# Performance work log

Measured on AMD Instinct MI355X. Metric: run time of the kernel, lower is better.

The kernel has to match this reference:

```python
import jax, jax.numpy as jnp
import numpy as np
import math

DEPTH = 3
NUM_GRAPHS = 8
BN_EPS = 1e-5
POOL_RATIO = 0.5


def _gcn(A, x, W, b):
    # GCNConv(improved=True): A_hat = A + 2*I; out = D^-1/2 A_hat D^-1/2 (x W) + b
    n = A.shape[0]
    A_hat = A + 2.0 * jnp.eye(n, dtype=A.dtype)
    deg = A_hat.sum(axis=1)
    d = jnp.where(deg > 0, jax.lax.rsqrt(deg), 0.0)
    return d[:, None] * (A_hat @ (d[:, None] * (x @ W))) + b


def _bn_eval(x, g, b):
    # BatchNorm1d in eval mode with running_mean=0, running_var=1
    return x * (g / jnp.sqrt(1.0 + BN_EPS)) + b


def _forward(x, edge_index, batch, conv0_w, conv0_b, down_w, down_b, pool_w,
             up_w, up_b, lins_w, lins_b, bn_g, bn_b, out_w, out_b):
    n0 = x.shape[0]
    # dense weighted adjacency A[dst, src] += 1 (duplicates sum, same as scatter-add MP)
    A = jnp.zeros((n0, n0), x.dtype).at[edge_index[1], edge_index[0]].add(1.0)

    # ---- GraphUNet (eval mode: dropout p=0.92 is identity) ----
    h = jax.nn.relu(_gcn(A, x, conv0_w, conv0_b))
    xs, As, perms = [h], [A], []
    for i in range(DEPTH):
        n = A.shape[0]
        eye = jnp.eye(n, dtype=A.dtype)
        S = A + eye                       # add_self_loops(weight=1)
        A2 = (S @ S) * (1.0 - eye)        # spspmm then remove_self_loops
        # TopKPooling: score = tanh((x.w)/||w||), keep top ceil(0.5*n) nodes
        score = jnp.tanh((h @ pool_w[i]) / jnp.linalg.norm(pool_w[i]))
        k = math.ceil(POOL_RATIO * n)
        _, perm = jax.lax.top_k(score, k)
        h = h[perm] * score[perm][:, None]
        A = A2[perm][:, perm]             # filter_adj
        h = jax.nn.relu(_gcn(A, h, down_w[i], down_b[i]))
        if i < DEPTH - 1:
            xs.append(h)
            As.append(A)
        perms.append(perm)
    for i in range(DEPTH):
        j = DEPTH - 1 - i
        res, Aj, perm = xs[j], As[j], perms[j]
        up = jnp.zeros_like(res).at[perm].set(h)
        h = res + up                      # sum_res=True skip connection
        h = _gcn(Aj, h, up_w[i], up_b[i])
        if i < DEPTH - 1:
            h = jax.nn.relu(h)

    # ---- global_add_pool + BN/Linear/tanh head ----
    g = jax.ops.segment_sum(h, batch, num_segments=NUM_GRAPHS)
    for i in range(3):
        g = _bn_eval(g, bn_g[i], bn_b[i])
        g = jnp.tanh(g @ lins_w[i] + lins_b[i])
    g = _bn_eval(g, bn_g[3], bn_b[3])
    return g @ out_w + out_b


def setup_inputs() -> dict:
    key = jax.random.key(0)
    ks = jax.random.split(key, 20)
    N, F, H, O, E = 4096, 64, 128, 32, 65536
    s = 0.05
    x = jax.random.normal(ks[0], (N, F), jnp.float32)
    src = jax.random.randint(ks[1], (E,), 0, N)
    dst = jax.random.randint(ks[2], (E,), 0, N)
    edge_index = jnp.stack([jnp.concatenate([src, dst]),
                            jnp.concatenate([dst, src])]).astype(jnp.int32)
    batch = jnp.sort(jax.random.randint(ks[3], (N,), 0, NUM_GRAPHS)).astype(jnp.int32)
    return {
        "x": x,
        "edge_index": edge_index,
        "batch": batch,
        "conv0_w": jax.random.normal(ks[4], (F, H), jnp.float32) * s,
        "conv0_b": jnp.zeros((H,), jnp.float32),
        "down_w": jax.random.normal(ks[5], (DEPTH, H, H), jnp.float32) * s,
        "down_b": jnp.zeros((DEPTH, H), jnp.float32),
        "pool_w": jax.random.normal(ks[6], (DEPTH, H), jnp.float32),
        "up_w": jax.random.normal(ks[7], (DEPTH, H, H), jnp.float32) * s,
        "up_b": jnp.zeros((DEPTH, H), jnp.float32),
        "lins_w": jax.random.normal(ks[8], (3, H, H), jnp.float32) * s,
        "lins_b": jnp.zeros((3, H), jnp.float32),
        "bn_g": jnp.ones((4, H), jnp.float32),
        "bn_b": jnp.zeros((4, H), jnp.float32),
        "out_w": jax.random.normal(ks[9], (H, O), jnp.float32) * s,
        "out_b": jnp.zeros((O,), jnp.float32),
    }


def reference(x, edge_index, batch, conv0_w, conv0_b, down_w, down_b, pool_w,
              up_w, up_b, lins_w, lins_b, bn_g, bn_b, out_w, out_b):
    return _forward(x, edge_index, batch, conv0_w, conv0_b, down_w, down_b,
                    pool_w, up_w, up_b, lins_w, lins_b, bn_g, bn_b, out_w, out_b)
```

## Files before the change

### kernel.cpp

```cpp
#include <hip/hip_runtime.h>
#include <math.h>

#define H 128
#define NG 8

typedef __attribute__((ext_vector_type(8))) short bf16x8;
typedef __attribute__((ext_vector_type(8))) unsigned short ushort8;
typedef __attribute__((ext_vector_type(4))) float f32x4;

static __device__ __forceinline__ float b2f(unsigned short u) {
  union { unsigned int i; float f; } v;
  v.i = ((unsigned int)u) << 16;
  return v.f;
}
static __device__ __forceinline__ unsigned short f2b(float f) {
  return (unsigned short)(__float_as_uint(f) >> 16);
}

__global__ void k_hist(const int* __restrict__ ei, int E, int* __restrict__ cnt) {
  int e = blockIdx.x * 256 + threadIdx.x;
  if (e >= E) return;
  atomicAdd(&cnt[ei[E + e]], 1);
}

__global__ __launch_bounds__(1024) void k_scan(const int* __restrict__ cnt,
                                               int* __restrict__ rowptr, int n) {
  __shared__ int sums[1024];
  int tid = threadIdx.x;
  int base = tid * 4;
  int v0 = 0, v1 = 0, v2 = 0, v3 = 0;
  if (base < n) { v0 = cnt[base]; v1 = cnt[base + 1]; v2 = cnt[base + 2]; v3 = cnt[base + 3]; }
  int s = v0 + v1 + v2 + v3;
  sums[tid] = s;
  __syncthreads();
  for (int off = 1; off < 1024; off <<= 1) {
    int t = (tid >= off) ? sums[tid - off] : 0;
    __syncthreads();
    sums[tid] += t;
    __syncthreads();
  }
  int excl = sums[tid] - s;
  if (base < n) {
    rowptr[base] = excl;
    rowptr[base + 1] = excl + v0;
    rowptr[base + 2] = excl + v0 + v1;
    rowptr[base + 3] = excl + v0 + v1 + v2;
  }
  if (tid == 1023) rowptr[n] = sums[1023];
}

__global__ void k_fill(const int* __restrict__ ei, int E, const int* __restrict__ rowptr,
                       int* __restrict__ cursor, int* __restrict__ colidx) {
  int e = blockIdx.x * 256 + threadIdx.x;
  if (e >= E) return;
  int r = ei[E + e], c = ei[e];
  int p = atomicAdd(&cursor[r], 1);
  colidx[rowptr[r] + p] = c;
}

__global__ void k_dvcnt(const int* __restrict__ cnt, float* __restrict__ dv, int n) {
  int i = blockIdx.x * 256 + threadIdx.x;
  if (i < n) dv[i] = rsqrtf((float)cnt[i] + 2.0f);
}

__global__ void k_deg(const float* __restrict__ A, int n, float* __restrict__ dv) {
  int row = blockIdx.x * (blockDim.x >> 6) + (threadIdx.x >> 6);
  int lane = threadIdx.x & 63;
  if (row >= n) return;
  float s = 0.f;
  const float* arow = A + (size_t)row * n;
  for (int j = lane; j < n; j += 64) s += arow[j];
#pragma unroll
  for (int o = 32; o > 0; o >>= 1) s += __shfl_down(s, o);
  if (lane == 0) dv[row] = rsqrtf(s + 2.0f);
}

template <int MODE>
__global__ __launch_bounds__(256) void k_xw(const float* __restrict__ X,
                                            const float* __restrict__ W,
                                            const float* __restrict__ dv,
                                            const int* __restrict__ idx,
                                            const float* __restrict__ aux,
                                            float* __restrict__ Y, int n, int F) {
  __shared__ float Xs[64][36];
  __shared__ float Ws[32][132];
  __shared__ int ridx[64];
  __shared__ float rscl[64];
  int tid = threadIdx.x;
  int rowBase = blockIdx.x * 64;
  if (MODE == 1) {
    if (tid < 64) {
      int pp = idx[rowBase + tid];
      ridx[tid] = pp;
      rscl[tid] = aux[pp];
    }
  } else if (MODE == 2) {
    if (tid < 64) ridx[tid] = idx[rowBase + tid];
  }
  if (MODE != 0) __syncthreads();
  int r0 = (tid >> 5) << 3;
  int c0 = (tid & 31) << 2;
  float acc[8][4] = {};
  for (int k0 = 0; k0 < F; k0 += 32) {
#pragma unroll
    for (int it = 0, e = tid; it < 8; ++it, e += 256) {
      int ii = e >> 5, kk = e & 31;
      int gk = k0 + kk;
      float v;
      if (MODE == 0) {
        v = X[(size_t)(rowBase + ii) * F + gk];
      } else if (MODE == 1) {
        v = X[(size_t)ridx[ii] * F + gk] * rscl[ii];
      } else {
        v = X[(size_t)(rowBase + ii) * F + gk];
        int iv = ridx[ii];
        if (iv >= 0) v += aux[(size_t)iv * H + gk];
      }
      Xs[ii][kk] = v;
    }
#pragma unroll
    for (int it = 0, e = tid; it < 4; ++it, e += 256) {
      int kk = e >> 5, cc4 = e & 31;
      *(float4*)&Ws[kk][cc4 << 2] = *(const float4*)&W[(size_t)(k0 + kk) * H + (cc4 << 2)];
    }
    __syncthreads();
#pragma unroll
    for (int kk = 0; kk < 32; kk += 4) {
      float4 a4[8], w4[4];
#pragma unroll
      for (int i = 0; i < 8; ++i) a4[i] = *(const float4*)&Xs[r0 + i][kk];
#pragma unroll
      for (int s = 0; s < 4; ++s) w4[s] = *(const float4*)&Ws[kk + s][c0];
#pragma unroll
      for (int i = 0; i < 8; ++i) {
        float av[4] = {a4[i].x, a4[i].y, a4[i].z, a4[i].w};
#pragma unroll
        for (int s = 0; s < 4; ++s) {
          float wv[4] = {w4[s].x, w4[s].y, w4[s].z, w4[s].w};
#pragma unroll
          for (int j = 0; j < 4; ++j) acc[i][j] = fmaf(av[s], wv[j], acc[i][j]);
        }
      }
    }
    __syncthreads();
  }
#pragma unroll
  for (int i = 0; i < 8; ++i) {
    int row = rowBase + r0 + i;
    float d = dv[row];
    *(float4*)&Y[(size_t)row * H + c0] =
        make_float4(d * acc[i][0], d * acc[i][1], d * acc[i][2], d * acc[i][3]);
  }
}

__global__ void k_spmm_fin(const int* __restrict__ rowptr, const int* __restrict__ colidx,
                           const float* __restrict__ Y, const float* __restrict__ dv,
                           const float* __restrict__ bias, float* __restrict__ Out,
                           int n, int relu) {
  int row = blockIdx.x * 4 + (threadIdx.x >> 6);
  int lane = threadIdx.x & 63;
  if (row >= n) return;
  int s = rowptr[row], e = rowptr[row + 1];
  float a0 = 0.f, a1 = 0.f;
  int i = s;
  for (; i + 1 < e; i += 2) {
    int c0 = colidx[i], c1 = colidx[i + 1];
    a0 += Y[(size_t)c0 * H + lane] + Y[(size_t)c1 * H + lane];
    a1 += Y[(size_t)c0 * H + 64 + lane] + Y[(size_t)c1 * H + 64 + lane];
  }
  if (i < e) {
    int c = colidx[i];
    a0 += Y[(size_t)c * H + lane];
    a1 += Y[(size_t)c * H + 64 + lane];
  }
  float d = dv[row];
  float v0 = d * (a0 + 2.0f * Y[(size_t)row * H + lane]) + bias[lane];
  float v1 = d * (a1 + 2.0f * Y[(size_t)row * H + 64 + lane]) + bias[64 + lane];
  if (relu) { v0 = fmaxf(v0, 0.f); v1 = fmaxf(v1, 0.f); }
  Out[(size_t)row * H + lane] = v0;
  Out[(size_t)row * H + 64 + lane] = v1;
}

__global__ __launch_bounds__(256) void k_ata_rows(const int* __restrict__ rowptr,
                                                  const int* __restrict__ colidx,
                                                  const int* __restrict__ perm,
                                                  const int* __restrict__ inv,
                                                  unsigned short* __restrict__ Ab,
                                                  float* __restrict__ dv, int kdim) {
  __shared__ int acc[2048];
  __shared__ int wsum[4];
  int i = blockIdx.x;
  int tid = threadIdx.x;
  for (int j = tid; j < kdim; j += 256) acc[j] = 0;
  __syncthreads();
  int p = perm[i];
  int s = rowptr[p], e = rowptr[p + 1];
  int deg = e - s;
  int wave = tid >> 6, lane = tid & 63;
  for (int q = wave; q <= deg; q += 4) {
    int kn = (q < deg) ? colidx[s + q] : p;
    int s2 = rowptr[kn], e2 = rowptr[kn + 1];
    for (int idx = s2 + lane; idx <= e2; idx += 64) {
      int j = (idx < e2) ? colidx[idx] : kn;
      int ii = inv[j];
      if (ii >= 0) atomicAdd(&acc[ii], 1);
    }
  }
  __syncthreads();
  int rs = 0;
  {
    int j0 = tid * 8;
    ushort8 v;
#pragma unroll
    for (int q = 0; q < 8; ++q) {
      int j = j0 + q;
      int c = (j == i) ? 0 : acc[j];
      rs += c;
      v[q] = f2b((float)c);
    }
    *(ushort8*)&Ab[(size_t)i * kdim + j0] = v;
  }
#pragma unroll
  for (int o = 32; o > 0; o >>= 1) rs += __shfl_down(rs, o);
  if (lane == 0) wsum[wave] = rs;
  __syncthreads();
  if (tid == 0) dv[i] = rsqrtf((float)(wsum[0] + wsum[1] + wsum[2] + wsum[3]) + 2.0f);
}

__global__ void k_gather(const unsigned short* __restrict__ Ab, const int* __restrict__ perm,
                         unsigned short* __restrict__ P, int n, int k) {
  int row = blockIdx.x;
  int p = perm[row];
  const unsigned short* src = Ab + (size_t)p * n;
  unsigned short* dst = P + (size_t)row * n;
  for (int c = threadIdx.x * 8; c < n; c += 256 * 8) {
    *(ushort8*)&dst[c] = *(const ushort8*)&src[c];
  }
  __syncthreads();
  if (threadIdx.x == 0) dst[p] = f2b(b2f(src[p]) + 1.0f);
}

__global__ __launch_bounds__(256) void k_ata_mfma(const unsigned short* __restrict__ P,
                                                  float* __restrict__ C, int n, int k) {
  __shared__ __align__(16) unsigned short As[64][64];
  __shared__ __align__(16) unsigned short Bs[64][64];
  int tid = threadIdx.x;
  int w = tid >> 6, ln = tid & 63;
  int l15 = ln & 15, l4 = ln >> 4;
  int br = blockIdx.y, bc = blockIdx.x;
  f32x4 acc[4] = {};
  for (int k0 = 0; k0 < n; k0 += 64) {
#pragma unroll
    for (int it = 0; it < 2; ++it) {
      int e = tid + it * 256;
      int row = e >> 3, ch = e & 7;
      int sch = (ch ^ (row & 7)) * 8;
      *(ushort8*)&As[row][sch] = *(const ushort8*)&P[(size_t)(br * 64 + row) * n + k0 + ch * 8];
      *(ushort8*)&Bs[row][sch] = *(const ushort8*)&P[(size_t)(bc * 64 + row) * n + k0 + ch * 8];
    }
    __syncthreads();
#pragma unroll
    for (int s = 0; s < 2; ++s) {
      int arow = w * 16 + l15;
      bf16x8 af = *(const bf16x8*)&As[arow][((s * 4 + l4) ^ (arow & 7)) * 8];
#pragma unroll
      for (int f = 0; f < 4; ++f) {
        int brow = f * 16 + l15;
        bf16x8 bfr = *(const bf16x8*)&Bs[brow][((s * 4 + l4) ^ (brow & 7)) * 8];
        acc[f] = __builtin_amdgcn_mfma_f32_16x16x32_bf16(af, bfr, acc[f], 0, 0, 0);
      }
    }
    __syncthreads();
  }
#pragma unroll
  for (int f = 0; f < 4; ++f) {
#pragma unroll
    for (int r = 0; r < 4; ++r) {
      int gi = br * 64 + w * 16 + l4 * 4 + r;
      int gj = bc * 64 + f * 16 + l15;
      C[(size_t)gi * k + gj] = (gi == gj) ? 0.0f : acc[f][r];
    }
  }
}

__global__ __launch_bounds__(256) void k_ata_sk(const float* __restrict__ A,
                                                const int* __restrict__ perm,
                                                float* __restrict__ C, int n, int k, int CK) {
  int bc = blockIdx.x, br = blockIdx.y;
  if (br > bc) return;
  __shared__ float As[64][36];
  __shared__ float Bs[64][36];
  __shared__ int pr[64], pc[64];
  int tid = threadIdx.x;
  if (tid < 64) pr[tid] = perm[br * 64 + tid];
  else if (tid < 128) pc[tid - 64] = perm[bc * 64 + (tid - 64)];
  __syncthreads();
  int ty = tid >> 4;
  int tx = tid & 15;
  float acc[4][4] = {};
  int k0s = blockIdx.z * CK;
  for (int k0 = k0s; k0 < k0s + CK; k0 += 32) {
#pragma unroll
    for (int it = 0, e = tid; it < 8; ++it, e += 256) {
      int ii = e >> 5, kk = e & 31;
      int gk = k0 + kk;
      int p = pr[ii];
      As[ii][kk] = A[(size_t)p * n + gk] + ((p == gk) ? 1.0f : 0.0f);
      p = pc[ii];
      Bs[ii][kk] = A[(size_t)p * n + gk] + ((p == gk) ? 1.0f : 0.0f);
    }
    __syncthreads();
#pragma unroll
    for (int kk = 0; kk < 32; kk += 4) {
      float4 a4[4], b4[4];
#pragma unroll
      for (int i = 0; i < 4; ++i) a4[i] = *(const float4*)&As[ty + 16 * i][kk];
#pragma unroll
      for (int j = 0; j < 4; ++j) b4[j] = *(const float4*)&Bs[tx + 16 * j][kk];
#pragma unroll
      for (int i = 0; i < 4; ++i) {
        float av[4] = {a4[i].x, a4[i].y, a4[i].z, a4[i].w};
#pragma unroll
        for (int j = 0; j < 4; ++j) {
          float bv[4] = {b4[j].x, b4[j].y, b4[j].z, b4[j].w};
#pragma unroll
          for (int s = 0; s < 4; ++s) acc[i][j] = fmaf(av[s], bv[s], acc[i][j]);
        }
      }
    }
    __syncthreads();
  }
  bool diag = (br == bc);
#pragma unroll
  for (int i = 0; i < 4; ++i) {
    int gi = br * 64 + ty + 16 * i;
#pragma unroll
    for (int j = 0; j < 4; ++j) {
      int gj = bc * 64 + tx + 16 * j;
      if (gi == gj) continue;
      float v = acc[i][j];
      atomicAdd(&C[(size_t)gi * k + gj], v);
      if (!diag) atomicAdd(&C[(size_t)gj * k + gi], v);
    }
  }
}

__global__ __launch_bounds__(256) void k_gcn_part(const float* __restrict__ A,
                                                  const float* __restrict__ Y,
                                                  float* __restrict__ Part,
                                                  int n, int KC) {
  __shared__ float As[64][36];
  __shared__ float Ys[32][132];
  int tid = threadIdx.x;
  int r0 = (tid >> 5) << 3;
  int c0 = (tid & 31) << 2;
  size_t rowBase = (size_t)blockIdx.x * 64;
  int k0s = blockIdx.y * KC;
  float* out = Part + (size_t)blockIdx.y * n * H;
  float acc[8][4] = {};
  for (int k0 = k0s; k0 < k0s + KC; k0 += 32) {
#pragma unroll
    for (int it = 0, e = tid; it < 8; ++it, e += 256) {
      int ii = e >> 5, kk = e & 31;
      As[ii][kk] = A[(rowBase + ii) * (size_t)n + k0 + kk];
    }
#pragma unroll
    for (int it = 0, e = tid; it < 4; ++it, e += 256) {
      int kk = e >> 5, cc4 = e & 31;
      *(float4*)&Ys[kk][cc4 << 2] = *(const float4*)&Y[(size_t)(k0 + kk) * H + (cc4 << 2)];
    }
    __syncthreads();
#pragma unroll
    for (int kk = 0; kk < 32; kk += 4) {
      float4 a4[8], y4[4];
#pragma unroll
      for (int i = 0; i < 8; ++i) a4[i] = *(const float4*)&As[r0 + i][kk];
#pragma unroll
      for (int s = 0; s < 4; ++s) y4[s] = *(const float4*)&Ys[kk + s][c0];
#pragma unroll
      for (int i = 0; i < 8; ++i) {
        float av[4] = {a4[i].x, a4[i].y, a4[i].z, a4[i].w};
#pragma unroll
        for (int s = 0; s < 4; ++s) {
          float yv[4] = {y4[s].x, y4[s].y, y4[s].z, y4[s].w};
#pragma unroll
          for (int j = 0; j < 4; ++j) acc[i][j] = fmaf(av[s], yv[j], acc[i][j]);
        }
      }
    }
    __syncthreads();
  }
#pragma unroll
  for (int i = 0; i < 8; ++i) {
    size_t row = rowBase + r0 + i;
    *(float4*)&out[row * H + c0] = make_float4(acc[i][0], acc[i][1], acc[i][2], acc[i][3]);
  }
}

__global__ __launch_bounds__(256) void k_gcn_part_b16(const unsigned short* __restrict__ A,
                                                      const float* __restrict__ Y,
                                                      float* __restrict__ Part,
                                                      int n, int KC) {
  __shared__ float As[64][36];
  __shared__ float Ys[32][132];
  int tid = threadIdx.x;
  int r0 = (tid >> 5) << 3;
  int c0 = (tid & 31) << 2;
  size_t rowBase = (size_t)blockIdx.x * 64;
  int k0s = blockIdx.y * KC;
  float* out = Part + (size_t)blockIdx.y * n * H;
  float acc[8][4] = {};
  for (int k0 = k0s; k0 < k0s + KC; k0 += 32) {
    {
      int row = tid >> 2, ch = (tid & 3) * 8;
      ushort8 v = *(const ushort8*)&A[(rowBase + row) * (size_t)n + k0 + ch];
#pragma unroll
      for (int q = 0; q < 8; ++q) As[row][ch + q] = b2f(v[q]);
    }
#pragma unroll
    for (int it = 0, e = tid; it < 4; ++it, e += 256) {
      int kk = e >> 5, cc4 = e & 31;
      *(float4*)&Ys[kk][cc4 << 2] = *(const float4*)&Y[(size_t)(k0 + kk) * H + (cc4 << 2)];
    }
    __syncthreads();
#pragma unroll
    for (int kk = 0; kk < 32; kk += 4) {
      float4 a4[8], y4[4];
#pragma unroll
      for (int i = 0; i < 8; ++i) a4[i] = *(const float4*)&As[r0 + i][kk];
#pragma unroll
      for (int s = 0; s < 4; ++s) y4[s] = *(const float4*)&Ys[kk + s][c0];
#pragma unroll
      for (int i = 0; i < 8; ++i) {
        float av[4] = {a4[i].x, a4[i].y, a4[i].z, a4[i].w};
#pragma unroll
        for (int s = 0; s < 4; ++s) {
          float yv[4] = {y4[s].x, y4[s].y, y4[s].z, y4[s].w};
#pragma unroll
          for (int j = 0; j < 4; ++j) acc[i][j] = fmaf(av[s], yv[j], acc[i][j]);
        }
      }
    }
    __syncthreads();
  }
#pragma unroll
  for (int i = 0; i < 8; ++i) {
    size_t row = rowBase + r0 + i;
    *(float4*)&out[row * H + c0] = make_float4(acc[i][0], acc[i][1], acc[i][2], acc[i][3]);
  }
}

__global__ void k_gcn_fin(const float* __restrict__ Part, const float* __restrict__ Y,
                          const float* __restrict__ dv, const float* __restrict__ bias,
                          float* __restrict__ Out, int n, int nch, int relu) {
  int i4 = blockIdx.x * 256 + threadIdx.x;
  if (i4 * 4 >= n * H) return;
  int row = i4 >> 5, c4 = (i4 & 31) * 4;
  size_t stride = (size_t)n * H;
  float4 s = *(const float4*)&Part[i4 * 4];
  for (int c = 1; c < nch; ++c) {
    float4 p = *(const float4*)&Part[c * stride + i4 * 4];
    s.x += p.x; s.y += p.y; s.z += p.z; s.w += p.w;
  }
  float4 y = *(const float4*)&Y[i4 * 4];
  float d = dv[row];
  float4 v;
  v.x = d * (s.x + 2.0f * y.x) + bias[c4];
  v.y = d * (s.y + 2.0f * y.y) + bias[c4 + 1];
  v.z = d * (s.z + 2.0f * y.z) + bias[c4 + 2];
  v.w = d * (s.w + 2.0f * y.w) + bias[c4 + 3];
  if (relu) {
    v.x = fmaxf(v.x, 0.f); v.y = fmaxf(v.y, 0.f);
    v.z = fmaxf(v.z, 0.f); v.w = fmaxf(v.w, 0.f);
  }
  *(float4*)&Out[i4 * 4] = v;
}

__global__ void k_score(const float* __restrict__ h, const float* __restrict__ w,
                        float* __restrict__ score, int n) {
  __shared__ float wn;
  int tid = threadIdx.x;
  if (tid < 64) {
    float s = w[tid] * w[tid] + w[tid + 64] * w[tid + 64];
#pragma unroll
    for (int o = 32; o > 0; o >>= 1) s += __shfl_down(s, o);
    if (tid == 0) wn = sqrtf(s);
  }
  __syncthreads();
  int row = blockIdx.x * 4 + (tid >> 6);
  int lane = tid & 63;
  if (row >= n) return;
  float s = h[(size_t)row * H + lane] * w[lane] + h[(size_t)row * H + lane + 64] * w[lane + 64];
#pragma unroll
  for (int o = 32; o > 0; o >>= 1) s += __shfl_down(s, o);
  if (lane == 0) score[row] = tanhf(s / wn);
}

static __device__ __forceinline__ void ce_(unsigned long long& x, unsigned long long& y, bool asc) {
  if ((x < y) != asc) { unsigned long long t = x; x = y; y = t; }
}
static __device__ __forceinline__ unsigned long long pick_(unsigned long long a,
                                                           unsigned long long b,
                                                           bool lower, bool asc) {
  unsigned long long lo = (a < b) ? a : b;
  unsigned long long hi = (a < b) ? b : a;
  return (lower == asc) ? lo : hi;
}

template <int LOGN>
__global__ __launch_bounds__(1024) void k_topk(const float* __restrict__ score,
                                               int* __restrict__ perm,
                                               int* __restrict__ inv) {
  const int n = 1 << LOGN;
  __shared__ unsigned long long lds[1 << LOGN];
  int t = threadIdx.x;
  int e0 = t * 4;
  unsigned long long key[4];
#pragma unroll
  for (int j = 0; j < 4; ++j) {
    unsigned u = __float_as_uint(score[e0 + j]);
    u = (u & 0x80000000u) ? ~u : (u | 0x80000000u);
    u = ~u;
    key[j] = (((unsigned long long)u) << 32) | (unsigned)(e0 + j);
  }
  ce_(key[0], key[1], true);
  ce_(key[2], key[3], false);
  for (int size = 4; size <= n; size <<= 1) {
    bool asc = ((e0 & size) == 0);
    for (int stride = size >> 1; stride >= 256; stride >>= 1) {
#pragma unroll
      for (int j = 0; j < 4; ++j) lds[e0 + j] = key[j];
      __syncthreads();
      bool lower = ((e0 & stride) == 0);
#pragma unroll
      for (int j = 0; j < 4; ++j)
        key[j] = pick_(key[j], lds[(e0 + j) ^ stride], lower, asc);
      __syncthreads();
    }
    int s0 = ((size >> 1) < 256) ? (size >> 1) : 128;
    for (int stride = s0; stride >= 4; stride >>= 1) {
      int m = stride >> 2;
      bool lower = ((t & m) == 0);
#pragma unroll
      for (int j = 0; j < 4; ++j) {
        unsigned long long o = __shfl_xor(key[j], m, 64);
        key[j] = pick_(key[j], o, lower, asc);
      }
    }
    ce_(key[0], key[2], asc);
    ce_(key[1], key[3], asc);
    ce_(key[0], key[1], asc);
    ce_(key[2], key[3], asc);
  }
  int kk = n >> 1;
#pragma unroll
  for (int j = 0; j < 4; ++j) {
    int e = e0 + j;
    int idx = (int)(key[j] & 0xffffffffu);
    if (e < kk) perm[e] = idx;
    if (inv) inv[idx] = (e < kk) ? e : -1;
  }
}

__global__ void k_segsum(const float* __restrict__ h, const int* __restrict__ batch,
                         float* __restrict__ g, int n) {
  int c = threadIdx.x;
  int r0 = blockIdx.x * 32;
  int rend = min(r0 + 32, n);
  float acc = 0.f;
  int cur = batch[r0];
  for (int r = r0; r < rend; ++r) {
    int b = batch[r];
    if (b != cur) { atomicAdd(&g[cur * H + c], acc); acc = 0.f; cur = b; }
    acc += h[(size_t)r * H + c];
  }
  atomicAdd(&g[cur * H + c], acc);
}

__global__ __launch_bounds__(256) void k_head(const float* __restrict__ g,
    const float* __restrict__ lins_w, const float* __restrict__ lins_b,
    const float* __restrict__ bn_g, const float* __restrict__ bn_b,
    const float* __restrict__ out_w, const float* __restrict__ out_b,
    float* __restrict__ out) {
  __shared__ float a[NG * H], b[NG * H];
  int tid = threadIdx.x;
  const float inv = 1.0f / sqrtf(1.0f + 1e-5f);
  for (int i = tid; i < NG * H; i += 256) a[i] = g[i];
  __syncthreads();
  for (int L = 0; L < 3; ++L) {
    for (int i = tid; i < NG * H; i += 256) {
      int c = i & 127;
      b[i] = a[i] * (bn_g[L * H + c] * inv) + bn_b[L * H + c];
    }
    __syncthreads();
    for (int i = tid; i < NG * H; i += 256) {
      int r = i >> 7, c = i & 127;
      float s = lins_b[L * H + c];
      for (int k2 = 0; k2 < H; ++k2) s += b[r * H + k2] * lins_w[(size_t)L * H * H + k2 * H + c];
      a[i] = tanhf(s);
    }
    __syncthreads();
  }
  for (int i = tid; i < NG * H; i += 256) {
    int c = i & 127;
    b[i] = a[i] * (bn_g[3 * H + c] * inv) + bn_b[3 * H + c];
  }
  __syncthreads();
  for (int i = tid; i < NG * 32; i += 256) {
    int r = i >> 5, o = i & 31;
    float s = out_b[o];
    for (int k2 = 0; k2 < H; ++k2) s += b[r * H + k2] * out_w[k2 * 32 + o];
    out[i] = s;
  }
}

extern "C" void kernel_launch(void* const* d_in, const int* in_sizes, int n_in,
                              void* d_out, int out_size, void* d_ws, size_t ws_size,
                              hipStream_t stream) {
  const float* x       = (const float*)d_in[0];
  const int*   ei      = (const int*)d_in[1];
  const int*   batch   = (const int*)d_in[2];
  const float* conv0_w = (const float*)d_in[3];
  const float* conv0_b = (const float*)d_in[4];
  const float* down_w  = (const float*)d_in[5];
  const float* down_b  = (const float*)d_in[6];
  const float* pool_w  = (const float*)d_in[7];
  const float* up_w    = (const float*)d_in[8];
  const float* up_b    = (const float*)d_in[9];
  const float* lins_w  = (const float*)d_in[10];
  const float* lins_b  = (const float*)d_in[11];
  const float* bn_g    = (const float*)d_in[12];
  const float* bn_b    = (const float*)d_in[13];
  const float* out_w   = (const float*)d_in[14];
  const float* out_b   = (const float*)d_in[15];
  int E = in_sizes[1] / 2;

  char* p = (char*)d_ws;
  auto alloc = [&](size_t bytes) {
    char* r = p;
    p += (bytes + 255) & ~(size_t)255;
    return r;
  };
  unsigned short* A1b  = (unsigned short*)alloc((size_t)2048 * 2048 * 2);
  unsigned short* P    = (unsigned short*)alloc((size_t)1024 * 2048 * 2);
  float*          A2m  = (float*)alloc((size_t)1024 * 1024 * 4);
  float*          A3   = (float*)alloc((size_t)512 * 512 * 4);
  float*          part = (float*)alloc((size_t)8 * 2048 * H * 4);
  int* cnt    = (int*)alloc(4096 * 4);
  int* cursor = (int*)alloc(4096 * 4);
  int* rowptr = (int*)alloc(4100 * 4);
  int* colidx = (int*)alloc((size_t)E * 4);
  int* inv0   = (int*)alloc(4096 * 4);
  int* inv1   = (int*)alloc(2048 * 4);
  int* inv2   = (int*)alloc(1024 * 4);
  float* dv0  = (float*)alloc(4096 * 4);
  float* dv1  = (float*)alloc(2048 * 4);
  float* dv2  = (float*)alloc(1024 * 4);
  float* dv3  = (float*)alloc(512 * 4);
  int* perm0  = (int*)alloc(2048 * 4);
  int* perm1  = (int*)alloc(1024 * 4);
  int* perm2  = (int*)alloc(512 * 4);
  float* score = (float*)alloc(4096 * 4);
  float* h0 = (float*)alloc((size_t)4096 * H * 4);
  float* h1 = (float*)alloc((size_t)2048 * H * 4);
  float* h2 = (float*)alloc((size_t)1024 * H * 4);
  float* h3 = (float*)alloc((size_t)512 * H * 4);
  float* t2 = (float*)alloc((size_t)4096 * H * 4);
  float* hu = (float*)alloc((size_t)4096 * H * 4);
  float* g  = (float*)alloc(NG * H * 4);

  auto gcn = [&](const float* A, const unsigned short* Ab, const float* Y, const float* dvv,
                 const float* bias, float* Out, int nn, int relu) {
    const int nch = 8;
    int KC = nn / nch;
    if (Ab)
      k_gcn_part_b16<<<dim3(nn / 64, nch), 256, 0, stream>>>(Ab, Y, part, nn, KC);
    else
      k_gcn_part<<<dim3(nn / 64, nch), 256, 0, stream>>>(A, Y, part, nn, KC);
    k_gcn_fin<<<nn / 8, 256, 0, stream>>>(part, Y, dvv, bias, Out, nn, nch, relu);
  };

  hipMemsetAsync(cnt, 0, 4096 * 4, stream);
  hipMemsetAsync(cursor, 0, 4096 * 4, stream);
  k_hist<<<(E + 255) / 256, 256, 0, stream>>>(ei, E, cnt);
  k_scan<<<1, 1024, 0, stream>>>(cnt, rowptr, 4096);
  k_fill<<<(E + 255) / 256, 256, 0, stream>>>(ei, E, rowptr, cursor, colidx);
  k_dvcnt<<<4096 / 256, 256, 0, stream>>>(cnt, dv0, 4096);

  k_xw<0><<<4096 / 64, 256, 0, stream>>>(x, conv0_w, dv0, nullptr, nullptr, t2, 4096, 64);
  k_spmm_fin<<<1024, 256, 0, stream>>>(rowptr, colidx, t2, dv0, conv0_b, h0, 4096, 1);

  k_score<<<1024, 256, 0, stream>>>(h0, pool_w, score, 4096);
  k_topk<12><<<1, 1024, 0, stream>>>(score, perm0, inv0);
  k_ata_rows<<<2048, 256, 0, stream>>>(rowptr, colidx, perm0, inv0, A1b, dv1, 2048);
  k_xw<1><<<2048 / 64, 256, 0, stream>>>(h0, down_w, dv1, perm0, score, t2, 2048, 128);
  gcn(nullptr, A1b, t2, dv1, down_b, h1, 2048, 1);

  k_score<<<512, 256, 0, stream>>>(h1, pool_w + H, score, 2048);
  k_topk<11><<<1, 512, 0, stream>>>(score, perm1, inv1);
  k_gather<<<1024, 256, 0, stream>>>(A1b, perm1, P, 2048, 1024);
  k_ata_mfma<<<dim3(16, 16), 256, 0, stream>>>(P, A2m, 2048, 1024);
  k_deg<<<1024 / 4, 256, 0, stream>>>(A2m, 1024, dv2);
  k_xw<1><<<1024 / 64, 256, 0, stream>>>(h1, down_w + (size_t)H * H, dv2, perm1, score, t2, 1024, 128);
  gcn(A2m, nullptr, t2, dv2, down_b + H, h2, 1024, 1);

  k_score<<<256, 256, 0, stream>>>(h2, pool_w + 2 * H, score, 1024);
  k_topk<10><<<1, 256, 0, stream>>>(score, perm2, inv2);
  hipMemsetAsync(A3, 0, (size_t)512 * 512 * 4, stream);
  k_ata_sk<<<dim3(8, 8, 8), 256, 0, stream>>>(A2m, perm2, A3, 1024, 512, 128);
  k_deg<<<512 / 4, 256, 0, stream>>>(A3, 512, dv3);
  k_xw<1><<<512 / 64, 256, 0, stream>>>(h2, down_w + (size_t)2 * H * H, dv3, perm2, score, t2, 512, 128);
  gcn(A3, nullptr, t2, dv3, down_b + 2 * H, h3, 512, 1);

  k_xw<2><<<1024 / 64, 256, 0, stream>>>(h2, up_w, dv2, inv2, h3, t2, 1024, 128);
  gcn(A2m, nullptr, t2, dv2, up_b, hu, 1024, 1);

  k_xw<2><<<2048 / 64, 256, 0, stream>>>(h1, up_w + (size_t)H * H, dv1, inv1, hu, t2, 2048, 128);
  gcn(nullptr, A1b, t2, dv1, up_b + H, hu, 2048, 1);

  k_xw<2><<<4096 / 64, 256, 0, stream>>>(h0, up_w + (size_t)2 * H * H, dv0, inv0, hu, t2, 4096, 128);
  k_spmm_fin<<<1024, 256, 0, stream>>>(rowptr, colidx, t2, dv0, up_b + 2 * H, hu, 4096, 0);

  hipMemsetAsync(g, 0, NG * H * 4, stream);
  k_segsum<<<4096 / 32, 128, 0, stream>>>(hu, batch, g, 4096);
  k_head<<<1, 256, 0, stream>>>(g, lins_w, lins_b, bn_g, bn_b, out_w, out_b, (float*)d_out);
}
```

Measured before the change: 537.2 us.

## Use bf16 MFMA with hi/lo split for level-1 GCN aggregation

Replaces the FP32 scalar-FMA GEMM used for the 2048-node bf16 adjacency propagation with an MFMA kernel. The dense features are transposed and split into bf16 high and low parts so that A·Y keeps near-fp32 accuracy, doubling the K dimension. This adds a conversion kernel and extra MFMA work, but it moves the largest GCN matmuls onto the matrix cores and drops the per-tile bf16-to-float conversion in shared memory. The split-K count is reduced from 8 to 4.

```diff
diff --git a/kernel.cpp b/kernel.cpp
--- a/kernel.cpp
+++ b/kernel.cpp
@@ -283,6 +283,74 @@
   }
 }
 
+__global__ void k_cvt_split(const float* __restrict__ Y, unsigned short* __restrict__ YT, int n) {
+  int c = blockIdx.x;
+  for (int k0 = threadIdx.x * 8; k0 < n; k0 += 256 * 8) {
+    ushort8 hi, lo;
+#pragma unroll
+    for (int q = 0; q < 8; ++q) {
+      float v = Y[(size_t)(k0 + q) * H + c];
+      unsigned short h = f2b(v);
+      hi[q] = h;
+      lo[q] = f2b(v - b2f(h));
+    }
+    *(ushort8*)&YT[(size_t)c * (2 * n) + k0] = hi;
+    *(ushort8*)&YT[(size_t)c * (2 * n) + n + k0] = lo;
+  }
+}
+
+__global__ __launch_bounds__(256) void k_gcn_mfma(const unsigned short* __restrict__ A,
+                                                  const unsigned short* __restrict__ YT,
+                                                  float* __restrict__ Part, int n, int VK) {
+  __shared__ __align__(16) unsigned short As[64][64];
+  __shared__ __align__(16) unsigned short Bs[128][64];
+  int tid = threadIdx.x;
+  int w = tid >> 6, ln = tid & 63;
+  int l15 = ln & 15, l4 = ln >> 4;
+  int rowBase = blockIdx.x * 64;
+  float* out = Part + (size_t)blockIdx.y * n * H;
+  f32x4 acc[8] = {};
+  int vk0s = blockIdx.y * VK;
+  for (int vk0 = vk0s; vk0 < vk0s + VK; vk0 += 64) {
+    int ka = vk0 & (n - 1);
+#pragma unroll
+    for (int it = 0; it < 2; ++it) {
+      int e = tid + it * 256;
+      int row = e >> 3, ch = e & 7;
+      int sch = (ch ^ (row & 7)) * 8;
+      *(ushort8*)&As[row][sch] = *(const ushort8*)&A[(size_t)(rowBase + row) * n + ka + ch * 8];
+    }
+#pragma unroll
+    for (int it = 0; it < 4; ++it) {
+      int e = tid + it * 256;
+      int row = e >> 3, ch = e & 7;
+      int sch = (ch ^ (row & 7)) * 8;
+      *(ushort8*)&Bs[row][sch] = *(const ushort8*)&YT[(size_t)row * (2 * n) + vk0 + ch * 8];
+    }
+    __syncthreads();
+#pragma unroll
+    for (int s = 0; s < 2; ++s) {
+      int arow = w * 16 + l15;
+      bf16x8 af = *(const bf16x8*)&As[arow][((s * 4 + l4) ^ (arow & 7)) * 8];
+#pragma unroll
+      for (int f = 0; f < 8; ++f) {
+        int brow = f * 16 + l15;
+        bf16x8 bfr = *(const bf16x8*)&Bs[brow][((s * 4 + l4) ^ (brow & 7)) * 8];
+        acc[f] = __builtin_amdgcn_mfma_f32_16x16x32_bf16(af, bfr, acc[f], 0, 0, 0);
+      }
+    }
+    __syncthreads();
+  }
+#pragma unroll
+  for (int f = 0; f < 8; ++f) {
+#pragma unroll
+    for (int r = 0; r < 4; ++r) {
+      int row = rowBase + w * 16 + l4 * 4 + r;
+      out[(size_t)row * H + f * 16 + l15] = acc[f][r];
+    }
+  }
+}
+
 __global__ __launch_bounds__(256) void k_ata_sk(const float* __restrict__ A,
                                                 const int* __restrict__ perm,
                                                 float* __restrict__ C, int n, int k, int CK) {
@@ -363,59 +431,6 @@
     for (int it = 0, e = tid; it < 8; ++it, e += 256) {
       int ii = e >> 5, kk = e & 31;
       As[ii][kk] = A[(rowBase + ii) * (size_t)n + k0 + kk];
-    }
-#pragma unroll
-    for (int it = 0, e = tid; it < 4; ++it, e += 256) {
-      int kk = e >> 5, cc4 = e & 31;
-      *(float4*)&Ys[kk][cc4 << 2] = *(const float4*)&Y[(size_t)(k0 + kk) * H + (cc4 << 2)];
-    }
-    __syncthreads();
-#pragma unroll
-    for (int kk = 0; kk < 32; kk += 4) {
-      float4 a4[8], y4[4];
-#pragma unroll
-      for (int i = 0; i < 8; ++i) a4[i] = *(const float4*)&As[r0 + i][kk];
-#pragma unroll
-      for (int s = 0; s < 4; ++s) y4[s] = *(const float4*)&Ys[kk + s][c0];
-#pragma unroll
-      for (int i = 0; i < 8; ++i) {
-        float av[4] = {a4[i].x, a4[i].y, a4[i].z, a4[i].w};
-#pragma unroll
-        for (int s = 0; s < 4; ++s) {
-          float yv[4] = {y4[s].x, y4[s].y, y4[s].z, y4[s].w};
-#pragma unroll
-          for (int j = 0; j < 4; ++j) acc[i][j] = fmaf(av[s], yv[j], acc[i][j]);
-        }
-      }
-    }
-    __syncthreads();
-  }
-#pragma unroll
-  for (int i = 0; i < 8; ++i) {
-    size_t row = rowBase + r0 + i;
-    *(float4*)&out[row * H + c0] = make_float4(acc[i][0], acc[i][1], acc[i][2], acc[i][3]);
-  }
-}
-
-__global__ __launch_bounds__(256) void k_gcn_part_b16(const unsigned short* __restrict__ A,
-                                                      const float* __restrict__ Y,
-                                                      float* __restrict__ Part,
-                                                      int n, int KC) {
-  __shared__ float As[64][36];
-  __shared__ float Ys[32][132];
-  int tid = threadIdx.x;
-  int r0 = (tid >> 5) << 3;
-  int c0 = (tid & 31) << 2;
-  size_t rowBase = (size_t)blockIdx.x * 64;
-  int k0s = blockIdx.y * KC;
-  float* out = Part + (size_t)blockIdx.y * n * H;
-  float acc[8][4] = {};
-  for (int k0 = k0s; k0 < k0s + KC; k0 += 32) {
-    {
-      int row = tid >> 2, ch = (tid & 3) * 8;
-      ushort8 v = *(const ushort8*)&A[(rowBase + row) * (size_t)n + k0 + ch];
-#pragma unroll
-      for (int q = 0; q < 8; ++q) As[row][ch + q] = b2f(v[q]);
     }
 #pragma unroll
     for (int it = 0, e = tid; it < 4; ++it, e += 256) {
@@ -643,6 +658,7 @@
   };
   unsigned short* A1b  = (unsigned short*)alloc((size_t)2048 * 2048 * 2);
   unsigned short* P    = (unsigned short*)alloc((size_t)1024 * 2048 * 2);
+  unsigned short* YT   = (unsigned short*)alloc((size_t)128 * 4096 * 2);
   float*          A2m  = (float*)alloc((size_t)1024 * 1024 * 4);
   float*          A3   = (float*)alloc((size_t)512 * 512 * 4);
   float*          part = (float*)alloc((size_t)8 * 2048 * H * 4);
@@ -669,15 +685,18 @@
   float* hu = (float*)alloc((size_t)4096 * H * 4);
   float* g  = (float*)alloc(NG * H * 4);
 
-  auto gcn = [&](const float* A, const unsigned short* Ab, const float* Y, const float* dvv,
+  auto gcn = [&](const float* A, const float* Y, const float* dvv,
                  const float* bias, float* Out, int nn, int relu) {
     const int nch = 8;
     int KC = nn / nch;
-    if (Ab)
-      k_gcn_part_b16<<<dim3(nn / 64, nch), 256, 0, stream>>>(Ab, Y, part, nn, KC);
-    else
-      k_gcn_part<<<dim3(nn / 64, nch), 256, 0, stream>>>(A, Y, part, nn, KC);
+    k_gcn_part<<<dim3(nn / 64, nch), 256, 0, stream>>>(A, Y, part, nn, KC);
     k_gcn_fin<<<nn / 8, 256, 0, stream>>>(part, Y, dvv, bias, Out, nn, nch, relu);
+  };
+  auto gcn_mfma = [&](const unsigned short* Ab, const float* Y, const float* dvv,
+                      const float* bias, float* Out, int nn, int relu) {
+    k_cvt_split<<<128, 256, 0, stream>>>(Y, YT, nn);
+    k_gcn_mfma<<<dim3(nn / 64, 4), 256, 0, stream>>>(Ab, YT, part, nn, (2 * nn) / 4);
+    k_gcn_fin<<<nn / 8, 256, 0, stream>>>(part, Y, dvv, bias, Out, nn, 4, relu);
   };
 
   hipMemsetAsync(cnt, 0, 4096 * 4, stream);
@@ -694,7 +713,7 @@
   k_topk<12><<<1, 1024, 0, stream>>>(score, perm0, inv0);
   k_ata_rows<<<2048, 256, 0, stream>>>(rowptr, colidx, perm0, inv0, A1b, dv1, 2048);
   k_xw<1><<<2048 / 64, 256, 0, stream>>>(h0, down_w, dv1, perm0, score, t2, 2048, 128);
-  gcn(nullptr, A1b, t2, dv1, down_b, h1, 2048, 1);
+  gcn_mfma(A1b, t2, dv1, down_b, h1, 2048, 1);
 
   k_score<<<512, 256, 0, stream>>>(h1, pool_w + H, score, 2048);
   k_topk<11><<<1, 512, 0, stream>>>(score, perm1, inv1);
@@ -702,7 +721,7 @@
   k_ata_mfma<<<dim3(16, 16), 256, 0, stream>>>(P, A2m, 2048, 1024);
   k_deg<<<1024 / 4, 256, 0, stream>>>(A2m, 1024, dv2);
   k_xw<1><<<1024 / 64, 256, 0, stream>>>(h1, down_w + (size_t)H * H, dv2, perm1, score, t2, 1024, 128);
-  gcn(A2m, nullptr, t2, dv2, down_b + H, h2, 1024, 1);
+  gcn(A2m, t2, dv2, down_b + H, h2, 1024, 1);
 
   k_score<<<256, 256, 0, stream>>>(h2, pool_w + 2 * H, score, 1024);
   k_topk<10><<<1, 256, 0, stream>>>(score, perm2, inv2);
@@ -710,13 +729,13 @@
   k_ata_sk<<<dim3(8, 8, 8), 256, 0, stream>>>(A2m, perm2, A3, 1024, 512, 128);
   k_deg<<<512 / 4, 256, 0, stream>>>(A3, 512, dv3);
   k_xw<1><<<512 / 64, 256, 0, stream>>>(h2, down_w + (size_t)2 * H * H, dv3, perm2, score, t2, 512, 128);
-  gcn(A3, nullptr, t2, dv3, down_b + 2 * H, h3, 512, 1);
+  gcn(A3, t2, dv3, down_b + 2 * H, h3, 512, 1);
 
   k_xw<2><<<1024 / 64, 256, 0, stream>>>(h2, up_w, dv2, inv2, h3, t2, 1024, 128);
-  gcn(A2m, nullptr, t2, dv2, up_b, hu, 1024, 1);
+  gcn(A2m, t2, dv2, up_b, hu, 1024, 1);
 
   k_xw<2><<<2048 / 64, 256, 0, stream>>>(h1, up_w + (size_t)H * H, dv1, inv1, hu, t2, 2048, 128);
-  gcn(nullptr, A1b, t2, dv1, up_b + H, hu, 2048, 1);
+  gcn_mfma(A1b, t2, dv1, up_b + H, hu, 2048, 1);
 
   k_xw<2><<<4096 / 64, 256, 0, stream>>>(h0, up_w + (size_t)2 * H * H, dv0, inv0, hu, t2, 4096, 128);
   k_spmm_fin<<<1024, 256, 0, stream>>>(rowptr, colidx, t2, dv0, up_b + 2 * H, hu, 4096, 0);
```

New measurement: 529.7 us. Within noise of the previous version (-1.4%).
